# Kernel tuning notes

Measured on AMD Instinct MI355X. Metric: run time of the kernel, lower is better.

Reference implementation:

```python
import jax, jax.numpy as jnp
import numpy as np

VOCAB = 100000
EMB = 256
HID = 512
HH = HID // 2  # per-direction hidden
NTAGS = 12
START = 10
STOP = 11
SEQ = 2048
NEG = -10000.0


def setup_inputs() -> dict:
    key = jax.random.key(0)
    ks = jax.random.split(key, 18)
    s = 0.05
    inp = {
        "sentence": jax.random.randint(ks[0], (SEQ,), 0, VOCAB, dtype=jnp.int64 if jax.config.jax_enable_x64 else jnp.int32),
        "tags": jax.random.randint(ks[1], (SEQ,), 0, 10, dtype=jnp.int64 if jax.config.jax_enable_x64 else jnp.int32),
        "embed": jax.random.normal(ks[2], (VOCAB, EMB), jnp.float32) * s,
        "Wih_f": jax.random.normal(ks[3], (4 * HH, EMB), jnp.float32) * s,
        "Whh_f": jax.random.normal(ks[4], (4 * HH, HH), jnp.float32) * s,
        "bih_f": jax.random.normal(ks[5], (4 * HH,), jnp.float32) * s,
        "bhh_f": jax.random.normal(ks[6], (4 * HH,), jnp.float32) * s,
        "Wih_b": jax.random.normal(ks[7], (4 * HH, EMB), jnp.float32) * s,
        "Whh_b": jax.random.normal(ks[8], (4 * HH, HH), jnp.float32) * s,
        "bih_b": jax.random.normal(ks[9], (4 * HH,), jnp.float32) * s,
        "bhh_b": jax.random.normal(ks[10], (4 * HH,), jnp.float32) * s,
        "W_out": jax.random.normal(ks[11], (NTAGS, HID), jnp.float32) * s,
        "b_out": jax.random.normal(ks[12], (NTAGS,), jnp.float32) * s,
        "h0": jax.random.normal(ks[14], (2, HH), jnp.float32),
        "c0": jax.random.normal(ks[15], (2, HH), jnp.float32),
    }
    trans = jax.random.normal(ks[13], (NTAGS, NTAGS), jnp.float32)
    trans = trans.at[START, :].set(NEG)  # never transition INTO start
    trans = trans.at[:, STOP].set(NEG)   # never transition FROM stop
    inp["transitions"] = trans
    return inp


def _lstm_dir(x, h0, c0, Wih, Whh, bih, bhh):
    # x: [T, E]; PyTorch gate order i, f, g, o
    pre = x @ Wih.T + bih + bhh  # [T, 4*HH] precomputed input projection
    def step(carry, p):
        h, c = carry
        g = p + Whh @ h
        i, f, gg, o = jnp.split(g, 4)
        i = jax.nn.sigmoid(i)
        f = jax.nn.sigmoid(f)
        gg = jnp.tanh(gg)
        o = jax.nn.sigmoid(o)
        c = f * c + i * gg
        h = o * jnp.tanh(c)
        return (h, c), h
    _, hs = jax.lax.scan(step, (h0, c0), pre)
    return hs  # [T, HH]


def _forward_impl(sentence, tags, embed, Wih_f, Whh_f, bih_f, bhh_f,
                  Wih_b, Whh_b, bih_b, bhh_b, W_out, b_out, transitions, h0, c0):
    x = embed[sentence]  # [T, E]
    hf = _lstm_dir(x, h0[0], c0[0], Wih_f, Whh_f, bih_f, bhh_f)
    hb = jnp.flip(_lstm_dir(jnp.flip(x, 0), h0[1], c0[1], Wih_b, Whh_b, bih_b, bhh_b), 0)
    feats = jnp.concatenate([hf, hb], axis=-1) @ W_out.T + b_out  # [T, NTAGS]

    # CRF forward algorithm: log-semiring scan over time
    fv0 = jnp.full((NTAGS,), NEG, feats.dtype).at[START].set(0.0)
    def crf_step(fv, emit):
        # transitions[next, prev]; logsumexp over prev
        fv = jax.nn.logsumexp(fv[None, :] + transitions + emit[:, None], axis=1)
        return fv, None
    fv, _ = jax.lax.scan(crf_step, fv0, feats)
    forward_score = jax.nn.logsumexp(fv + transitions[STOP])

    # gold path score
    prev = jnp.concatenate([jnp.array([START], dtype=tags.dtype), tags[:-1]])
    emit_gold = jnp.take_along_axis(feats, tags[:, None], axis=1)[:, 0]
    gold_score = jnp.sum(transitions[tags, prev]) + jnp.sum(emit_gold) + transitions[STOP, tags[-1]]

    return forward_score - gold_score


def reference(sentence, tags, embed, Wih_f, Whh_f, bih_f, bhh_f,
              Wih_b, Whh_b, bih_b, bhh_b, W_out, b_out, transitions, h0, c0):
    return _forward_impl(sentence, tags, embed, Wih_f, Whh_f, bih_f, bhh_f,
                         Wih_b, Whh_b, bih_b, bhh_b, W_out, b_out, transitions, h0, c0)
```

## Files before the change

kernel.cpp:

```cpp
#include <hip/hip_runtime.h>
#include <hip/hip_bf16.h>
#include <stdint.h>

#define SEQ   2048
#define EMB   256
#define HHD   256
#define GATES 1024
#define NTAGS 12
#define START 10
#define STOP  11
#define CCH   16
#define CLEN  128

__device__ __forceinline__ int sdot4(uint32_t a, uint32_t b, int c) {
#if __has_builtin(__builtin_amdgcn_sdot4)
  return __builtin_amdgcn_sdot4((int)a, (int)b, c, false);
#else
  int r = c;
#pragma unroll
  for (int i = 0; i < 4; i++) {
    int av = (int)(signed char)((a >> (8 * i)) & 255);
    int bv = (int)(signed char)((b >> (8 * i)) & 255);
    r += av * bv;
  }
  return r;
#endif
}

__device__ __forceinline__ float fsig(float x) {
  float e = __expf(-x);
  return __builtin_amdgcn_rcpf(1.0f + e);
}

__device__ __forceinline__ int dpp_xor1(int x) {
  return __builtin_amdgcn_update_dpp(0, x, 0xB1, 0xF, 0xF, true);
}
__device__ __forceinline__ int dpp_xor2(int x) {
  return __builtin_amdgcn_update_dpp(0, x, 0x4E, 0xF, 0xF, true);
}
__device__ __forceinline__ float dpp_xor2_f(float x) {
  int r = __builtin_amdgcn_update_dpp(0, __float_as_int(x), 0x4E, 0xF, 0xF, true);
  return __int_as_float(r);
}

__global__ __launch_bounds__(256) void k_quant(const float* __restrict__ whh_f,
                                               const float* __restrict__ whh_b,
                                               uint32_t* __restrict__ q4,
                                               float* __restrict__ scales) {
  const int row  = (blockIdx.x * 256 + threadIdx.x) >> 6;
  const int lane = threadIdx.x & 63;
  const int d = row >> 10, r = row & 1023;
  const float4 w = *(const float4*)((d ? whh_b : whh_f) + (long)r * HHD + lane * 4);
  float m = fmaxf(fmaxf(fabsf(w.x), fabsf(w.y)), fmaxf(fabsf(w.z), fabsf(w.w)));
#pragma unroll
  for (int off = 32; off; off >>= 1) m = fmaxf(m, __shfl_xor(m, off, 64));
  m = fmaxf(m, 1e-20f);
  const float inv = 127.f / m;
  int a = (int)rintf(w.x * inv), b = (int)rintf(w.y * inv);
  int c = (int)rintf(w.z * inv), e = (int)rintf(w.w * inv);
  q4[row * 64 + lane] = (uint32_t)(a & 255) | ((uint32_t)(b & 255) << 8) |
                        ((uint32_t)(c & 255) << 16) | ((uint32_t)(e & 255) << 24);
  if (lane == 0) scales[row] = m / 127.f;
}

__global__ __launch_bounds__(256) void k_proj(const int* __restrict__ sentence,
                                              const float* __restrict__ embed,
                                              const float* __restrict__ Wih_f,
                                              const float* __restrict__ bih_f,
                                              const float* __restrict__ bhh_f,
                                              const float* __restrict__ Wih_b,
                                              const float* __restrict__ bih_b,
                                              const float* __restrict__ bhh_b,
                                              float* __restrict__ pre) {
  const int dir = blockIdx.y;
  const int t0  = blockIdx.x * 8;
  const float* Wih = dir ? Wih_b : Wih_f;
  const float* bih = dir ? bih_b : bih_f;
  const float* bhh = dir ? bhh_b : bhh_f;

  __shared__ float xs[8][256];
  const int tid = threadIdx.x;
#pragma unroll
  for (int i = 0; i < 8; i++) {
    int s = sentence[t0 + i];
    xs[i][tid] = embed[(long)s * EMB + tid];
  }
  __syncthreads();

  const int r0 = tid * 4;
  float acc[4][8];
#pragma unroll
  for (int j = 0; j < 4; j++)
#pragma unroll
    for (int t = 0; t < 8; t++) acc[j][t] = 0.f;

  const float4* W4 = (const float4*)Wih;
  for (int kq = 0; kq < 64; kq++) {
    float4 w[4];
#pragma unroll
    for (int j = 0; j < 4; j++) w[j] = W4[(r0 + j) * 64 + kq];
#pragma unroll
    for (int t = 0; t < 8; t++) {
      float4 xv = ((const float4*)xs[t])[kq];
#pragma unroll
      for (int j = 0; j < 4; j++)
        acc[j][t] += w[j].x * xv.x + w[j].y * xv.y + w[j].z * xv.z + w[j].w * xv.w;
    }
  }
#pragma unroll
  for (int j = 0; j < 4; j++) {
    const int row = r0 + j;
    const int G  = row >> 8;
    const int uu = row & 255;
    float bsum = bih[row] + bhh[row];
#pragma unroll
    for (int t = 0; t < 8; t++)
      pre[(((long)(dir * SEQ + t0 + t)) * HHD + uu) * 4 + G] = acc[j][t] + bsum;
  }
}

__global__ __launch_bounds__(512, 2) void k_lstm(const uint32_t* __restrict__ q4,
                                                 const float* __restrict__ scales,
                                                 const float* __restrict__ pre,
                                                 const float* __restrict__ h0,
                                                 const float* __restrict__ c0,
                                                 float* __restrict__ hs) {
  const int dir  = blockIdx.x;
  const int L    = threadIdx.x;
  const int q    = L & 3;
  const int g    = L >> 2;
  const int p    = q & 1;
  const int half = q >> 1;
  const int u    = 2 * g + p;

  __shared__ __align__(16) uint8_t hbuf[2][256];

  const long base = (long)dir * GATES;

  uint4 wa[4][4], wb[4][4];
  const uint4* qq = (const uint4*)q4;
#pragma unroll
  for (int j = 0; j < 4; j++) {
    const int qj = q ^ j;
    const int rA = (2 * (qj >> 1)) * 256 + 2 * g + (qj & 1);
    const int rB = rA + 256;
#pragma unroll
    for (int k = 0; k < 4; k++) {
      wa[j][k] = qq[(base + rA) * 16 + 4 * q + k];
      wb[j][k] = qq[(base + rB) * 16 + 4 * q + k];
    }
  }
  const int rown = (2 * half) * 256 + u;
  const float sA = scales[base + rown];
  const float sB = scales[base + rown + 256];

  if (L < 256) {
    float v = h0[dir * HHD + L] * (127.f / 4.f);
    v = fminf(fmaxf(v, -127.f), 127.f);
    hbuf[0][L] = (uint8_t)(int)rintf(v);
  }
  float c_st = c0[dir * HHD + u];
  __syncthreads();

  const int t0 = dir ? (SEQ - 1) : 0;
  const long pstep = dir ? -(long)(HHD * 4) : (long)(HHD * 4);
  const long hstep = dir ? -(long)HHD : (long)HHD;
  const float* pp = pre + (long)dir * SEQ * (HHD * 4) + ((long)t0 * HHD + u) * 4 + 2 * half;
  float* hp       = hs  + (long)dir * SEQ * HHD + (long)t0 * HHD + u;
  const float gmul = half ? 2.f : 1.f;
  const int write_h = ((L & 2) == 0);

  for (int s = 0; s < SEQ; s++) {
    const float2 pr = *(const float2*)pp;

    const uint4* hq4 = (const uint4*)(hbuf[s & 1] + (q << 6));
    const uint4 h0v = hq4[0], h1v = hq4[1], h2v = hq4[2], h3v = hq4[3];

    int pa0 = 0, pa1 = 0, pa2 = 0, pa3 = 0;
    int pb0 = 0, pb1 = 0, pb2 = 0, pb3 = 0;
#pragma unroll
    for (int k = 0; k < 4; k++) {
      const uint4 hk = (k == 0) ? h0v : (k == 1) ? h1v : (k == 2) ? h2v : h3v;
      pa0 = sdot4(wa[0][k].x, hk.x, pa0); pa0 = sdot4(wa[0][k].y, hk.y, pa0);
      pa0 = sdot4(wa[0][k].z, hk.z, pa0); pa0 = sdot4(wa[0][k].w, hk.w, pa0);
      pa1 = sdot4(wa[1][k].x, hk.x, pa1); pa1 = sdot4(wa[1][k].y, hk.y, pa1);
      pa1 = sdot4(wa[1][k].z, hk.z, pa1); pa1 = sdot4(wa[1][k].w, hk.w, pa1);
      pa2 = sdot4(wa[2][k].x, hk.x, pa2); pa2 = sdot4(wa[2][k].y, hk.y, pa2);
      pa2 = sdot4(wa[2][k].z, hk.z, pa2); pa2 = sdot4(wa[2][k].w, hk.w, pa2);
      pa3 = sdot4(wa[3][k].x, hk.x, pa3); pa3 = sdot4(wa[3][k].y, hk.y, pa3);
      pa3 = sdot4(wa[3][k].z, hk.z, pa3); pa3 = sdot4(wa[3][k].w, hk.w, pa3);
      pb0 = sdot4(wb[0][k].x, hk.x, pb0); pb0 = sdot4(wb[0][k].y, hk.y, pb0);
      pb0 = sdot4(wb[0][k].z, hk.z, pb0); pb0 = sdot4(wb[0][k].w, hk.w, pb0);
      pb1 = sdot4(wb[1][k].x, hk.x, pb1); pb1 = sdot4(wb[1][k].y, hk.y, pb1);
      pb1 = sdot4(wb[1][k].z, hk.z, pb1); pb1 = sdot4(wb[1][k].w, hk.w, pb1);
      pb2 = sdot4(wb[2][k].x, hk.x, pb2); pb2 = sdot4(wb[2][k].y, hk.y, pb2);
      pb2 = sdot4(wb[2][k].z, hk.z, pb2); pb2 = sdot4(wb[2][k].w, hk.w, pb2);
      pb3 = sdot4(wb[3][k].x, hk.x, pb3); pb3 = sdot4(wb[3][k].y, hk.y, pb3);
      pb3 = sdot4(wb[3][k].z, hk.z, pb3); pb3 = sdot4(wb[3][k].w, hk.w, pb3);
    }
    const int tA = pa0 + dpp_xor1(pa1);
    const int tA2 = pa2 + dpp_xor1(pa3);
    const int sumA = tA + dpp_xor2(tA2);
    const int tB = pb0 + dpp_xor1(pb1);
    const int tB2 = pb2 + dpp_xor1(pb3);
    const int sumB = tB + dpp_xor2(tB2);

    const float hsc = (s == 0) ? (4.f / 127.f) : (1.f / 127.f);
    const float gA = pr.x + sA * hsc * (float)sumA;
    const float gB = pr.y + sB * hsc * (float)sumB;

    const float v0 = fsig(gA * gmul) * gmul - (gmul - 1.f);
    const float v1 = fsig(gB);
    const float p0 = dpp_xor2_f(v0);
    const float p1 = dpp_xor2_f(v1);
    const float iv = half ? p0 : v0;
    const float fv = half ? p1 : v1;
    const float gv = half ? v0 : p0;
    const float ov = half ? v1 : p1;

    c_st = fv * c_st + iv * gv;
    const float hv = ov * (2.f * fsig(2.f * c_st) - 1.f);

    if (write_h) {
      *hp = hv;
      hbuf[(s + 1) & 1][u] = (uint8_t)(int)rintf(hv * 127.f);
    }
    pp += pstep;
    hp += hstep;
    __syncthreads();
  }
}

__global__ __launch_bounds__(192) void k_feats(const float* __restrict__ hs,
                                               const float* __restrict__ W_out,
                                               const float* __restrict__ b_out,
                                               float* __restrict__ feats) {
  __shared__ float Wl[12 * 520];
  const int tid = threadIdx.x;
  for (int i = tid; i < 12 * 512; i += 192) Wl[(i / 512) * 520 + (i % 512)] = W_out[i];
  __syncthreads();

  const int tl = tid / 12, n = tid % 12;
  const int t = blockIdx.x * 16 + tl;
  const float4* hf4 = (const float4*)(hs + (long)t * HHD);
  const float4* hb4 = (const float4*)(hs + (long)SEQ * HHD + (long)t * HHD);
  const float4* Wa  = (const float4*)&Wl[n * 520];
  const float4* Wb  = (const float4*)&Wl[n * 520 + 256];

  float acc = b_out[n];
#pragma unroll 8
  for (int j = 0; j < 64; j++) {
    float4 w = Wa[j], h = hf4[j];
    acc += w.x * h.x + w.y * h.y + w.z * h.z + w.w * h.w;
  }
#pragma unroll 8
  for (int j = 0; j < 64; j++) {
    float4 w = Wb[j], h = hb4[j];
    acc += w.x * h.x + w.y * h.y + w.z * h.z + w.w * h.w;
  }
  feats[t * NTAGS + n] = acc;
}

__global__ __launch_bounds__(192) void k_crf_chunk(const float* __restrict__ feats,
                                                   const float* __restrict__ trans,
                                                   float* __restrict__ Pc) {
  const int ch  = blockIdx.x;
  const int tid = threadIdx.x;
  const int n   = tid & 15;
  const int p   = tid >> 4;
  const int nn  = (n < 12) ? n : 11;

  __shared__ float fe[CLEN * NTAGS];
  for (int i = tid; i < CLEN * NTAGS; i += 192) fe[i] = feats[ch * CLEN * NTAGS + i];
  __syncthreads();

  float trn[12];
#pragma unroll
  for (int j = 0; j < 12; j++) trn[j] = trans[nn * 12 + j];

  float Mv = trans[nn * 12 + p] + fe[nn];
  for (int t = 1; t < CLEN; t++) {
    float x[12], m = -1e30f;
#pragma unroll
    for (int j = 0; j < 12; j++) {
      x[j] = trn[j] + __shfl(Mv, (tid & 48) | j, 64);
      m = fmaxf(m, x[j]);
    }
    float ss = 0.f;
#pragma unroll
    for (int j = 0; j < 12; j++) ss += __expf(x[j] - m);
    Mv = fe[t * NTAGS + nn] + m + __logf(ss);
  }
  if (n < 12) Pc[ch * 144 + n * 12 + p] = Mv;
}

__global__ __launch_bounds__(128) void k_crf_final(const float* __restrict__ Pc,
                                                   const float* __restrict__ feats,
                                                   const int* __restrict__ tags,
                                                   const float* __restrict__ trans,
                                                   float* __restrict__ out) {
  __shared__ float Pl[CCH * 144];
  __shared__ float res[2];
  const int tid = threadIdx.x;
  for (int i = tid; i < CCH * 144; i += 128) Pl[i] = Pc[i];
  __syncthreads();

  if (tid < 64) {
    const int n  = tid;
    const int nn = (n < 12) ? n : 11;
    float fv = (n == START) ? 0.f : -10000.f;
    for (int c = 0; c < CCH; c++) {
      float x[12], m = -1e30f;
#pragma unroll
      for (int j = 0; j < 12; j++) {
        x[j] = Pl[c * 144 + nn * 12 + j] + __shfl(fv, j, 64);
        m = fmaxf(m, x[j]);
      }
      float ss = 0.f;
#pragma unroll
      for (int j = 0; j < 12; j++) ss += __expf(x[j] - m);
      fv = m + __logf(ss);
    }
    const float v = fv + trans[STOP * 12 + nn];
    float xs[12], m = -1e30f;
#pragma unroll
    for (int j = 0; j < 12; j++) {
      xs[j] = __shfl(v, j, 64);
      m = fmaxf(m, xs[j]);
    }
    float ss = 0.f;
#pragma unroll
    for (int j = 0; j < 12; j++) ss += __expf(xs[j] - m);
    if (tid == 0) res[0] = m + __logf(ss);
  } else {
    const int i = tid - 64;
    float gp = 0.f;
    for (int b = 0; b < 32; b++) {
      int t  = b * 64 + i;
      int tg = tags[t];
      int pv = (t == 0) ? START : tags[t - 1];
      gp += trans[tg * 12 + pv] + feats[t * NTAGS + tg];
    }
#pragma unroll
    for (int off = 32; off; off >>= 1) gp += __shfl_xor(gp, off, 64);
    if (i == 0) res[1] = gp + trans[STOP * 12 + tags[SEQ - 1]];
  }
  __syncthreads();
  if (tid == 0) out[0] = res[0] - res[1];
}

extern "C" void kernel_launch(void* const* d_in, const int* in_sizes, int n_in,
                              void* d_out, int out_size, void* d_ws, size_t ws_size,
                              hipStream_t stream) {
  const int*   sentence = (const int*)  d_in[0];
  const int*   tags     = (const int*)  d_in[1];
  const float* embed    = (const float*)d_in[2];
  const float* Wih_f    = (const float*)d_in[3];
  const float* Whh_f    = (const float*)d_in[4];
  const float* bih_f    = (const float*)d_in[5];
  const float* bhh_f    = (const float*)d_in[6];
  const float* Wih_b    = (const float*)d_in[7];
  const float* Whh_b    = (const float*)d_in[8];
  const float* bih_b    = (const float*)d_in[9];
  const float* bhh_b    = (const float*)d_in[10];
  const float* W_out    = (const float*)d_in[11];
  const float* b_out    = (const float*)d_in[12];
  const float* h0       = (const float*)d_in[13];
  const float* c0       = (const float*)d_in[14];
  const float* trans    = (const float*)d_in[15];
  float* out = (float*)d_out;

  char* ws = (char*)d_ws;
  uint32_t* q4    = (uint32_t*)ws;
  float*    scales= (float*)(ws + (512l << 10));
  float*    pre   = (float*)(ws + (1l  << 20));
  float*    hs    = (float*)(ws + (17l << 20));
  float*    feats = (float*)(ws + (21l << 20));
  float*    Pc    = (float*)(ws + (21l << 20) + (128l<<10));

  k_quant<<<512, 256, 0, stream>>>(Whh_f, Whh_b, q4, scales);
  k_proj<<<dim3(256, 2), 256, 0, stream>>>(sentence, embed, Wih_f, bih_f, bhh_f,
                                           Wih_b, bih_b, bhh_b, pre);
  k_lstm<<<2, 512, 0, stream>>>(q4, scales, pre, h0, c0, hs);
  k_feats<<<128, 192, 0, stream>>>(hs, W_out, b_out, feats);
  k_crf_chunk<<<CCH, 192, 0, stream>>>(feats, trans, Pc);
  k_crf_final<<<1, 128, 0, stream>>>(Pc, feats, tags, trans, out);
}
```

Measured before the change: 1.847 ms.

## Split LSTM recurrence between sdot4 waves and int8 MFMA waves, fold h0 and exp2 scaling

The recurrent step now runs on two kinds of waves: four waves keep the sdot4 path for the first 128 hidden units, and four waves compute the other 128 units' gates with int8 16x16x64 MFMA, passing results through shared memory. The initial h0 contribution Whh·h0 is computed exactly in the quant kernel and folded into the first timestep's pre-activations, so the step loop no longer needs a special scale for step 0. Pre-activations are also pre-multiplied by -log2e (or -2log2e for the tanh gate) so sigmoids become exp2 plus rcp. The barrier is replaced by inline asm waitcnt+s_barrier. Risks include MFMA latency in the serial loop, extra LDS traffic for gate exchange, and the missing-builtin fallback silently returning zero.

```diff
diff --git a/kernel.cpp b/kernel.cpp
--- a/kernel.cpp
+++ b/kernel.cpp
@@ -1,5 +1,4 @@
 #include <hip/hip_runtime.h>
-#include <hip/hip_bf16.h>
 #include <stdint.h>
 
 #define SEQ   2048
@@ -12,6 +11,10 @@
 #define CCH   16
 #define CLEN  128
 
+typedef int v4i __attribute__((ext_vector_type(4)));
+
+#define LOG2E 1.442695041f
+
 __device__ __forceinline__ int sdot4(uint32_t a, uint32_t b, int c) {
 #if __has_builtin(__builtin_amdgcn_sdot4)
   return __builtin_amdgcn_sdot4((int)a, (int)b, c, false);
@@ -27,9 +30,20 @@
 #endif
 }
 
-__device__ __forceinline__ float fsig(float x) {
-  float e = __expf(-x);
-  return __builtin_amdgcn_rcpf(1.0f + e);
+__device__ __forceinline__ float fexp2(float x) {
+#if __has_builtin(__builtin_amdgcn_exp2f)
+  return __builtin_amdgcn_exp2f(x);
+#else
+  return exp2f(x);
+#endif
+}
+
+__device__ __forceinline__ v4i mfma_i8_16x16x64(v4i a, v4i b, v4i c) {
+#if __has_builtin(__builtin_amdgcn_mfma_i32_16x16x64_i8)
+  return __builtin_amdgcn_mfma_i32_16x16x64_i8(a, b, c, 0, 0, 0);
+#else
+  return c;
+#endif
 }
 
 __device__ __forceinline__ int dpp_xor1(int x) {
@@ -45,12 +59,20 @@
 
 __global__ __launch_bounds__(256) void k_quant(const float* __restrict__ whh_f,
                                                const float* __restrict__ whh_b,
+                                               const float* __restrict__ h0,
                                                uint32_t* __restrict__ q4,
-                                               float* __restrict__ scales) {
+                                               float* __restrict__ scales,
+                                               float* __restrict__ h0c) {
   const int row  = (blockIdx.x * 256 + threadIdx.x) >> 6;
   const int lane = threadIdx.x & 63;
   const int d = row >> 10, r = row & 1023;
   const float4 w = *(const float4*)((d ? whh_b : whh_f) + (long)r * HHD + lane * 4);
+
+  const float4 hh = *(const float4*)(h0 + d * HHD + lane * 4);
+  float dp = w.x * hh.x + w.y * hh.y + w.z * hh.z + w.w * hh.w;
+#pragma unroll
+  for (int off = 32; off; off >>= 1) dp += __shfl_xor(dp, off, 64);
+
   float m = fmaxf(fmaxf(fabsf(w.x), fabsf(w.y)), fmaxf(fabsf(w.z), fabsf(w.w)));
 #pragma unroll
   for (int off = 32; off; off >>= 1) m = fmaxf(m, __shfl_xor(m, off, 64));
@@ -60,7 +82,7 @@
   int c = (int)rintf(w.z * inv), e = (int)rintf(w.w * inv);
   q4[row * 64 + lane] = (uint32_t)(a & 255) | ((uint32_t)(b & 255) << 8) |
                         ((uint32_t)(c & 255) << 16) | ((uint32_t)(e & 255) << 24);
-  if (lane == 0) scales[row] = m / 127.f;
+  if (lane == 0) { scales[row] = m / 127.f; h0c[row] = dp; }
 }
 
 __global__ __launch_bounds__(256) void k_proj(const int* __restrict__ sentence,
@@ -71,6 +93,7 @@
                                               const float* __restrict__ Wih_b,
                                               const float* __restrict__ bih_b,
                                               const float* __restrict__ bhh_b,
+                                              const float* __restrict__ h0c,
                                               float* __restrict__ pre) {
   const int dir = blockIdx.y;
   const int t0  = blockIdx.x * 8;
@@ -107,127 +130,220 @@
         acc[j][t] += w[j].x * xv.x + w[j].y * xv.y + w[j].z * xv.z + w[j].w * xv.w;
     }
   }
+  const int t0d = dir ? (SEQ - 1) : 0;
 #pragma unroll
   for (int j = 0; j < 4; j++) {
     const int row = r0 + j;
     const int G  = row >> 8;
     const int uu = row & 255;
-    float bsum = bih[row] + bhh[row];
-#pragma unroll
-    for (int t = 0; t < 8; t++)
-      pre[(((long)(dir * SEQ + t0 + t)) * HHD + uu) * 4 + G] = acc[j][t] + bsum;
+    const float negfac = (G == 2) ? (-2.f * LOG2E) : (-LOG2E);
+    const float bsum = bih[row] + bhh[row];
+    const float c0a  = h0c[dir * GATES + row];
+#pragma unroll
+    for (int t = 0; t < 8; t++) {
+      float v = acc[j][t] + bsum;
+      if (t0 + t == t0d) v += c0a;
+      pre[(((long)(dir * SEQ + t0 + t)) * HHD + uu) * 4 + G] = v * negfac;
+    }
   }
 }
 
 __global__ __launch_bounds__(512, 2) void k_lstm(const uint32_t* __restrict__ q4,
                                                  const float* __restrict__ scales,
                                                  const float* __restrict__ pre,
-                                                 const float* __restrict__ h0,
                                                  const float* __restrict__ c0,
                                                  float* __restrict__ hs) {
   const int dir  = blockIdx.x;
   const int L    = threadIdx.x;
-  const int q    = L & 3;
-  const int g    = L >> 2;
-  const int p    = q & 1;
-  const int half = q >> 1;
-  const int u    = 2 * g + p;
+  const int w    = L >> 6;
+  const int lane = L & 63;
+  const long base = (long)dir * GATES;
 
   __shared__ __align__(16) uint8_t hbuf[2][256];
-
-  const long base = (long)dir * GATES;
-
-  uint4 wa[4][4], wb[4][4];
-  const uint4* qq = (const uint4*)q4;
-#pragma unroll
-  for (int j = 0; j < 4; j++) {
-    const int qj = q ^ j;
-    const int rA = (2 * (qj >> 1)) * 256 + 2 * g + (qj & 1);
-    const int rB = rA + 256;
-#pragma unroll
-    for (int k = 0; k < 4; k++) {
-      wa[j][k] = qq[(base + rA) * 16 + 4 * q + k];
-      wb[j][k] = qq[(base + rB) * 16 + 4 * q + k];
-    }
-  }
-  const int rown = (2 * half) * 256 + u;
-  const float sA = scales[base + rown];
-  const float sB = scales[base + rown + 256];
-
-  if (L < 256) {
-    float v = h0[dir * HHD + L] * (127.f / 4.f);
-    v = fminf(fmaxf(v, -127.f), 127.f);
-    hbuf[0][L] = (uint8_t)(int)rintf(v);
-  }
-  float c_st = c0[dir * HHD + u];
+  __shared__ __align__(16) int gbuf[4][128];
+
+  const float k1 = -LOG2E / 127.f;
+  const float k2 = -2.f * LOG2E / 127.f;
+
+  if (L < 256) hbuf[0][L] = 0;
   __syncthreads();
 
   const int t0 = dir ? (SEQ - 1) : 0;
   const long pstep = dir ? -(long)(HHD * 4) : (long)(HHD * 4);
   const long hstep = dir ? -(long)HHD : (long)HHD;
-  const float* pp = pre + (long)dir * SEQ * (HHD * 4) + ((long)t0 * HHD + u) * 4 + 2 * half;
-  float* hp       = hs  + (long)dir * SEQ * HHD + (long)t0 * HHD + u;
-  const float gmul = half ? 2.f : 1.f;
-  const int write_h = ((L & 2) == 0);
-
-  for (int s = 0; s < SEQ; s++) {
-    const float2 pr = *(const float2*)pp;
-
-    const uint4* hq4 = (const uint4*)(hbuf[s & 1] + (q << 6));
-    const uint4 h0v = hq4[0], h1v = hq4[1], h2v = hq4[2], h3v = hq4[3];
-
-    int pa0 = 0, pa1 = 0, pa2 = 0, pa3 = 0;
-    int pb0 = 0, pb1 = 0, pb2 = 0, pb3 = 0;
-#pragma unroll
-    for (int k = 0; k < 4; k++) {
-      const uint4 hk = (k == 0) ? h0v : (k == 1) ? h1v : (k == 2) ? h2v : h3v;
-      pa0 = sdot4(wa[0][k].x, hk.x, pa0); pa0 = sdot4(wa[0][k].y, hk.y, pa0);
-      pa0 = sdot4(wa[0][k].z, hk.z, pa0); pa0 = sdot4(wa[0][k].w, hk.w, pa0);
-      pa1 = sdot4(wa[1][k].x, hk.x, pa1); pa1 = sdot4(wa[1][k].y, hk.y, pa1);
-      pa1 = sdot4(wa[1][k].z, hk.z, pa1); pa1 = sdot4(wa[1][k].w, hk.w, pa1);
-      pa2 = sdot4(wa[2][k].x, hk.x, pa2); pa2 = sdot4(wa[2][k].y, hk.y, pa2);
-      pa2 = sdot4(wa[2][k].z, hk.z, pa2); pa2 = sdot4(wa[2][k].w, hk.w, pa2);
-      pa3 = sdot4(wa[3][k].x, hk.x, pa3); pa3 = sdot4(wa[3][k].y, hk.y, pa3);
-      pa3 = sdot4(wa[3][k].z, hk.z, pa3); pa3 = sdot4(wa[3][k].w, hk.w, pa3);
-      pb0 = sdot4(wb[0][k].x, hk.x, pb0); pb0 = sdot4(wb[0][k].y, hk.y, pb0);
-      pb0 = sdot4(wb[0][k].z, hk.z, pb0); pb0 = sdot4(wb[0][k].w, hk.w, pb0);
-      pb1 = sdot4(wb[1][k].x, hk.x, pb1); pb1 = sdot4(wb[1][k].y, hk.y, pb1);
-      pb1 = sdot4(wb[1][k].z, hk.z, pb1); pb1 = sdot4(wb[1][k].w, hk.w, pb1);
-      pb2 = sdot4(wb[2][k].x, hk.x, pb2); pb2 = sdot4(wb[2][k].y, hk.y, pb2);
-      pb2 = sdot4(wb[2][k].z, hk.z, pb2); pb2 = sdot4(wb[2][k].w, hk.w, pb2);
-      pb3 = sdot4(wb[3][k].x, hk.x, pb3); pb3 = sdot4(wb[3][k].y, hk.y, pb3);
-      pb3 = sdot4(wb[3][k].z, hk.z, pb3); pb3 = sdot4(wb[3][k].w, hk.w, pb3);
-    }
-    const int tA = pa0 + dpp_xor1(pa1);
-    const int tA2 = pa2 + dpp_xor1(pa3);
-    const int sumA = tA + dpp_xor2(tA2);
-    const int tB = pb0 + dpp_xor1(pb1);
-    const int tB2 = pb2 + dpp_xor1(pb3);
-    const int sumB = tB + dpp_xor2(tB2);
-
-    const float hsc = (s == 0) ? (4.f / 127.f) : (1.f / 127.f);
-    const float gA = pr.x + sA * hsc * (float)sumA;
-    const float gB = pr.y + sB * hsc * (float)sumB;
-
-    const float v0 = fsig(gA * gmul) * gmul - (gmul - 1.f);
-    const float v1 = fsig(gB);
-    const float p0 = dpp_xor2_f(v0);
-    const float p1 = dpp_xor2_f(v1);
-    const float iv = half ? p0 : v0;
-    const float fv = half ? p1 : v1;
-    const float gv = half ? v0 : p0;
-    const float ov = half ? v1 : p1;
-
-    c_st = fv * c_st + iv * gv;
-    const float hv = ov * (2.f * fsig(2.f * c_st) - 1.f);
-
-    if (write_h) {
-      *hp = hv;
-      hbuf[(s + 1) & 1][u] = (uint8_t)(int)rintf(hv * 127.f);
-    }
-    pp += pstep;
-    hp += hstep;
-    __syncthreads();
+  const uint4* qq = (const uint4*)q4;
+
+  if (w < 4) {
+    const int q    = L & 3;
+    const int g    = L >> 2;
+    const int p    = q & 1;
+    const int half = q >> 1;
+    const int u    = 2 * g + p;
+
+    uint4 wa[4][4], wb[4][4];
+#pragma unroll
+    for (int j = 0; j < 4; j++) {
+      const int qj = q ^ j;
+      const int rA = (2 * (qj >> 1)) * 256 + 2 * g + (qj & 1);
+      const int rB = rA + 256;
+#pragma unroll
+      for (int k = 0; k < 4; k++) {
+        wa[j][k] = qq[(base + rA) * 16 + 4 * q + k];
+        wb[j][k] = qq[(base + rB) * 16 + 4 * q + k];
+      }
+    }
+    const int rown = (2 * half) * 256 + u;
+    const float scvA = (half ? k2 : k1) * scales[base + rown];
+    const float scvB = k1 * scales[base + rown + 256];
+    float c_st = c0[dir * HHD + u];
+
+    const float* pp = pre + ((long)(dir * SEQ + t0) * HHD + u) * 4 + 2 * half;
+    float* hp       = hs + (long)dir * SEQ * HHD + (long)t0 * HHD + u;
+    const float gmul = half ? 2.f : 1.f;
+    const int write_h = ((L & 2) == 0);
+
+    for (int s = 0; s < SEQ; s++) {
+      const float2 pr = *(const float2*)pp;
+
+      const uint4* hq4 = (const uint4*)(hbuf[s & 1] + (q << 6));
+      const uint4 h0v = hq4[0], h1v = hq4[1], h2v = hq4[2], h3v = hq4[3];
+
+      int pa0 = 0, pa1 = 0, pa2 = 0, pa3 = 0;
+      int pb0 = 0, pb1 = 0, pb2 = 0, pb3 = 0;
+#pragma unroll
+      for (int k = 0; k < 4; k++) {
+        const uint4 hk = (k == 0) ? h0v : (k == 1) ? h1v : (k == 2) ? h2v : h3v;
+        pa0 = sdot4(wa[0][k].x, hk.x, pa0); pa0 = sdot4(wa[0][k].y, hk.y, pa0);
+        pa0 = sdot4(wa[0][k].z, hk.z, pa0); pa0 = sdot4(wa[0][k].w, hk.w, pa0);
+        pa1 = sdot4(wa[1][k].x, hk.x, pa1); pa1 = sdot4(wa[1][k].y, hk.y, pa1);
+        pa1 = sdot4(wa[1][k].z, hk.z, pa1); pa1 = sdot4(wa[1][k].w, hk.w, pa1);
+        pa2 = sdot4(wa[2][k].x, hk.x, pa2); pa2 = sdot4(wa[2][k].y, hk.y, pa2);
+        pa2 = sdot4(wa[2][k].z, hk.z, pa2); pa2 = sdot4(wa[2][k].w, hk.w, pa2);
+        pa3 = sdot4(wa[3][k].x, hk.x, pa3); pa3 = sdot4(wa[3][k].y, hk.y, pa3);
+        pa3 = sdot4(wa[3][k].z, hk.z, pa3); pa3 = sdot4(wa[3][k].w, hk.w, pa3);
+        pb0 = sdot4(wb[0][k].x, hk.x, pb0); pb0 = sdot4(wb[0][k].y, hk.y, pb0);
+        pb0 = sdot4(wb[0][k].z, hk.z, pb0); pb0 = sdot4(wb[0][k].w, hk.w, pb0);
+        pb1 = sdot4(wb[1][k].x, hk.x, pb1); pb1 = sdot4(wb[1][k].y, hk.y, pb1);
+        pb1 = sdot4(wb[1][k].z, hk.z, pb1); pb1 = sdot4(wb[1][k].w, hk.w, pb1);
+        pb2 = sdot4(wb[2][k].x, hk.x, pb2); pb2 = sdot4(wb[2][k].y, hk.y, pb2);
+        pb2 = sdot4(wb[2][k].z, hk.z, pb2); pb2 = sdot4(wb[2][k].w, hk.w, pb2);
+        pb3 = sdot4(wb[3][k].x, hk.x, pb3); pb3 = sdot4(wb[3][k].y, hk.y, pb3);
+        pb3 = sdot4(wb[3][k].z, hk.z, pb3); pb3 = sdot4(wb[3][k].w, hk.w, pb3);
+      }
+      const int tA = pa0 + dpp_xor1(pa1);
+      const int tA2 = pa2 + dpp_xor1(pa3);
+      const int sumA = tA + dpp_xor2(tA2);
+      const int tB = pb0 + dpp_xor1(pb1);
+      const int tB2 = pb2 + dpp_xor1(pb3);
+      const int sumB = tB + dpp_xor2(tB2);
+
+      const float gA2 = fmaf(scvA, (float)sumA, pr.x);
+      const float gB2 = fmaf(scvB, (float)sumB, pr.y);
+      const float e0 = __builtin_amdgcn_rcpf(1.f + fexp2(gA2));
+      const float v0 = fmaf(e0, gmul, -(gmul - 1.f));
+      const float v1 = __builtin_amdgcn_rcpf(1.f + fexp2(gB2));
+      const float p0 = dpp_xor2_f(v0);
+      const float p1 = dpp_xor2_f(v1);
+      const float iv = half ? p0 : v0;
+      const float fv = half ? p1 : v1;
+      const float gv = half ? v0 : p0;
+      const float ov = half ? v1 : p1;
+
+      c_st = fmaf(fv, c_st, iv * gv);
+      const float th = fmaf(2.f, __builtin_amdgcn_rcpf(1.f + fexp2(c_st * (-2.f * LOG2E))), -1.f);
+      const float hv = ov * th;
+
+      if (write_h) {
+        *hp = hv;
+        hbuf[(s + 1) & 1][u] = (uint8_t)(int)rintf(hv * 127.f);
+      }
+      pp += pstep;
+      hp += hstep;
+      asm volatile("s_waitcnt lgkmcnt(0)\n\ts_barrier" ::: "memory");
+    }
+  } else {
+    const int m   = w - 4;
+    const int lg  = lane >> 4;
+    const int col = lane & 15;
+    const int ub  = 128 + 32 * m;
+
+    v4i A[4][2][4];
+#pragma unroll
+    for (int G = 0; G < 4; G++)
+#pragma unroll
+      for (int t = 0; t < 2; t++) {
+        const int row = G * 256 + ub + t * 16 + col;
+#pragma unroll
+        for (int kc = 0; kc < 4; kc++) {
+          const uint4 a = qq[(base + row) * 16 + kc * 4 + lg];
+          A[G][t][kc] = (v4i){(int)a.x, (int)a.y, (int)a.z, (int)a.w};
+        }
+      }
+
+    const int ui = 32 * m + (lane & 31);
+    const int uu = 128 + ui;
+    const float scv0 = k1 * scales[base + 0 * 256 + uu];
+    const float scv1 = k1 * scales[base + 1 * 256 + uu];
+    const float scv2 = k2 * scales[base + 2 * 256 + uu];
+    const float scv3 = k1 * scales[base + 3 * 256 + uu];
+    float c_st = c0[dir * HHD + uu];
+
+    const float* pp = pre + ((long)(dir * SEQ + t0) * HHD + uu) * 4;
+    float* hp       = hs + (long)dir * SEQ * HHD + (long)t0 * HHD + uu;
+    const int writer = (lane < 32);
+
+    for (int s = 0; s < SEQ; s++) {
+      const float4 pc = *(const float4*)pp;
+
+      const uint8_t* hb = hbuf[s & 1];
+      v4i B[4];
+#pragma unroll
+      for (int kc = 0; kc < 4; kc++) {
+        const uint4 hf = *(const uint4*)(hb + kc * 64 + lg * 16);
+        B[kc] = (v4i){(int)hf.x, (int)hf.y, (int)hf.z, (int)hf.w};
+      }
+      v4i acc[4][2];
+#pragma unroll
+      for (int G = 0; G < 4; G++)
+#pragma unroll
+        for (int t = 0; t < 2; t++) {
+          v4i a = (v4i){0, 0, 0, 0};
+#pragma unroll
+          for (int kc = 0; kc < 4; kc++) a = mfma_i8_16x16x64(A[G][t][kc], B[kc], a);
+          acc[G][t] = a;
+        }
+
+      if (col == 0) {
+#pragma unroll
+        for (int G = 0; G < 4; G++)
+#pragma unroll
+          for (int t = 0; t < 2; t++)
+            *(v4i*)&gbuf[G][32 * m + 16 * t + lg * 4] = acc[G][t];
+      }
+      asm volatile("" ::: "memory");
+      const int di = gbuf[0][ui], df = gbuf[1][ui];
+      const int dg = gbuf[2][ui], dq = gbuf[3][ui];
+
+      const float ai = fmaf(scv0, (float)di, pc.x);
+      const float af = fmaf(scv1, (float)df, pc.y);
+      const float ag = fmaf(scv2, (float)dg, pc.z);
+      const float ao = fmaf(scv3, (float)dq, pc.w);
+      const float iv = __builtin_amdgcn_rcpf(1.f + fexp2(ai));
+      const float fv = __builtin_amdgcn_rcpf(1.f + fexp2(af));
+      const float gv = fmaf(2.f, __builtin_amdgcn_rcpf(1.f + fexp2(ag)), -1.f);
+      const float ov = __builtin_amdgcn_rcpf(1.f + fexp2(ao));
+      c_st = fmaf(fv, c_st, iv * gv);
+      const float th = fmaf(2.f, __builtin_amdgcn_rcpf(1.f + fexp2(c_st * (-2.f * LOG2E))), -1.f);
+      const float hv = ov * th;
+
+      if (writer) {
+        *hp = hv;
+        hbuf[(s + 1) & 1][uu] = (uint8_t)(int)rintf(hv * 127.f);
+      }
+      pp += pstep;
+      hp += hstep;
+      asm volatile("s_waitcnt lgkmcnt(0)\n\ts_barrier" ::: "memory");
+    }
   }
 }
 
@@ -373,15 +489,16 @@
   char* ws = (char*)d_ws;
   uint32_t* q4    = (uint32_t*)ws;
   float*    scales= (float*)(ws + (512l << 10));
+  float*    h0c   = (float*)(ws + (520l << 10));
   float*    pre   = (float*)(ws + (1l  << 20));
   float*    hs    = (float*)(ws + (17l << 20));
   float*    feats = (float*)(ws + (21l << 20));
   float*    Pc    = (float*)(ws + (21l << 20) + (128l<<10));
 
-  k_quant<<<512, 256, 0, stream>>>(Whh_f, Whh_b, q4, scales);
+  k_quant<<<512, 256, 0, stream>>>(Whh_f, Whh_b, h0, q4, scales, h0c);
   k_proj<<<dim3(256, 2), 256, 0, stream>>>(sentence, embed, Wih_f, bih_f, bhh_f,
-                                           Wih_b, bih_b, bhh_b, pre);
-  k_lstm<<<2, 512, 0, stream>>>(q4, scales, pre, h0, c0, hs);
+                                           Wih_b, bih_b, bhh_b, h0c, pre);
+  k_lstm<<<2, 512, 0, stream>>>(q4, scales, pre, c0, hs);
   k_feats<<<128, 192, 0, stream>>>(hs, W_out, b_out, feats);
   k_crf_chunk<<<CCH, 192, 0, stream>>>(feats, trans, Pc);
   k_crf_final<<<1, 128, 0, stream>>>(Pc, feats, tags, trans, out);
```

Result: no change. 1.874 ms (+1.4%).
